# Performance work log

Measured on AMD Instinct MI355X. Metric: run time of the kernel, lower is better.

## Reference

```python
import jax, jax.numpy as jnp
import numpy as np

ROPE_BASE = 100.0  # CroCo RoPE2D default freq


def _rope1d(tok, pos):
    # tok: [B, H, N, D], pos: [B, N] int
    D = tok.shape[-1]
    inv_freq = 1.0 / (ROPE_BASE ** (jnp.arange(0, D, 2, dtype=jnp.float32) / D))
    ang = pos[..., None].astype(jnp.float32) * inv_freq          # [B, N, D/2]
    cos = jnp.concatenate([jnp.cos(ang), jnp.cos(ang)], -1)[:, None]  # [B,1,N,D]
    sin = jnp.concatenate([jnp.sin(ang), jnp.sin(ang)], -1)[:, None]
    x1, x2 = jnp.split(tok, 2, axis=-1)
    rot = jnp.concatenate([-x2, x1], -1)
    return tok * cos.astype(tok.dtype) + rot * sin.astype(tok.dtype)


def _rope2d(tok, pos):
    # first half of head channels rotated with y coords, second half with x
    t_y, t_x = jnp.split(tok, 2, axis=-1)
    return jnp.concatenate([_rope1d(t_y, pos[..., 0]), _rope1d(t_x, pos[..., 1])], -1)


def setup_inputs() -> dict:
    key0 = jax.random.key(0)
    ks = jax.random.split(key0, 10)
    B, Nq, Nk, C, H = 4, 2048, 2048, 1024, 16
    s = 1.0 / np.sqrt(C)
    return {
        "query": jax.random.normal(ks[0], (B, Nq, C), jnp.float32),
        "key": jax.random.normal(ks[1], (B, Nk, C), jnp.float32),
        "value": jax.random.normal(ks[2], (B, Nk, C), jnp.float32),
        "qpos": jax.random.randint(ks[3], (B, Nq, 2), 0, 64),
        "kpos": jax.random.randint(ks[4], (B, Nk, 2), 0, 64),
        "Wq": jax.random.normal(ks[5], (C, C), jnp.float32) * s,
        "Wk": jax.random.normal(ks[6], (C, C), jnp.float32) * s,
        "Wv": jax.random.normal(ks[7], (C, C), jnp.float32) * s,
        "Wo": jax.random.normal(ks[8], (C, C), jnp.float32) * s,
        "bo": jax.random.normal(ks[9], (C,), jnp.float32) * 0.01,
    }


def reference(query, key, value, qpos, kpos, Wq, Wk, Wv, Wo, bo):
    B, Nq, C = query.shape
    H = 16
    D = C // H
    scale = D ** (-0.5)
    # separate Q/K/V projections (torch Linear: x @ W.T), split into heads
    q = (query @ Wq.T).reshape(B, Nq, H, D).transpose(0, 2, 1, 3)
    k = (key @ Wk.T).reshape(B, key.shape[1], H, D).transpose(0, 2, 1, 3)
    v = (value @ Wv.T).reshape(B, value.shape[1], H, D).transpose(0, 2, 1, 3)
    # inline fp16 cast around RoPE, as in the original
    q = _rope2d(q.astype(jnp.float16), qpos).astype(jnp.float32)
    k = _rope2d(k.astype(jnp.float16), kpos).astype(jnp.float32)
    # SDPA
    scores = jnp.einsum("bhqd,bhkd->bhqk", q, k) * scale
    attn = jax.nn.softmax(scores, axis=-1)
    x = jnp.einsum("bhqk,bhkd->bhqd", attn, v)
    x = x.transpose(0, 2, 1, 3).reshape(B, Nq, C)
    return x @ Wo.T + bo
```

## Files before the change

kernel.cpp:

```cpp
#include <hip/hip_runtime.h>
#include <math.h>

typedef _Float16 half_t;
typedef __attribute__((ext_vector_type(8))) _Float16 f16x8;
typedef __attribute__((ext_vector_type(4))) float f32x4;

#define MFMA16(a, b, c) __builtin_amdgcn_mfma_f32_16x16x32_f16((a), (b), (c), 0, 0, 0)

constexpr int Bc = 4, NQ = 2048, NKC = 2048, CC = 1024, NHD = 16, HDIM = 64;

__device__ __forceinline__ void async_copy16(half_t* lds, const half_t* g) {
  __builtin_amdgcn_global_load_lds(
      (const __attribute__((address_space(1))) unsigned*)g,
      (__attribute__((address_space(3))) unsigned*)lds, 16, 0, 0);
}

__global__ __launch_bounds__(256) void cvt16(const float* __restrict__ src,
                                             half_t* __restrict__ dst) {
  const int i = blockIdx.x * 256 + threadIdx.x;
  const f32x4 a = ((const f32x4*)src)[2 * i];
  const f32x4 b = ((const f32x4*)src)[2 * i + 1];
  f16x8 h;
#pragma unroll
  for (int j = 0; j < 4; ++j) { h[j] = (half_t)a[j]; h[4 + j] = (half_t)b[j]; }
  ((f16x8*)dst)[i] = h;
}

__global__ __launch_bounds__(256) void cvtW(const float* __restrict__ s0,
                                            const float* __restrict__ s1,
                                            const float* __restrict__ s2,
                                            const float* __restrict__ s3,
                                            half_t* __restrict__ dst) {
  const int y = blockIdx.y;
  const float* src = (y == 0) ? s0 : (y == 1) ? s1 : (y == 2) ? s2 : s3;
  const int i = blockIdx.x * 256 + threadIdx.x;
  const f32x4 a = ((const f32x4*)src)[2 * i];
  const f32x4 b = ((const f32x4*)src)[2 * i + 1];
  f16x8 h;
#pragma unroll
  for (int j = 0; j < 4; ++j) { h[j] = (half_t)a[j]; h[4 + j] = (half_t)b[j]; }
  ((f16x8*)(dst + (size_t)y * CC * CC))[i] = h;
}

template <bool FINAL>
__global__ __launch_bounds__(256) void gemm_lds(const half_t* __restrict__ X,
                                                const half_t* __restrict__ W,
                                                half_t* __restrict__ out16,
                                                float* __restrict__ outf,
                                                const float* __restrict__ bias) {
  __shared__ half_t As[128 * 32];
  __shared__ half_t Bs[128 * 32];
  const int tid  = threadIdx.x;
  const int wave = tid >> 6, lane = tid & 63;
  const int quad = lane >> 4, l16 = lane & 15;
  const int m0 = blockIdx.y * 128, n0 = blockIdx.x * 128;
  const int mw = (wave >> 1) * 64, nw = (wave & 1) * 64;

  const int srow = lane >> 2, skoff = (lane & 3) * 8;
  const half_t* xa = X + (size_t)(m0 + wave * 32 + srow) * CC + skoff;
  const half_t* xb = W + (size_t)(n0 + wave * 32 + srow) * CC + skoff;
  half_t* lA0 = &As[(wave * 2 + 0) * 512];
  half_t* lA1 = &As[(wave * 2 + 1) * 512];
  half_t* lB0 = &Bs[(wave * 2 + 0) * 512];
  half_t* lB1 = &Bs[(wave * 2 + 1) * 512];

  f32x4 acc[4][4] = {};

  for (int k0 = 0; k0 < CC; k0 += 32) {
    __syncthreads();
    async_copy16(lA0, xa + k0);
    async_copy16(lA1, xa + 16 * CC + k0);
    async_copy16(lB0, xb + k0);
    async_copy16(lB1, xb + 16 * CC + k0);
    __syncthreads();

    f16x8 af[4], bf[4];
#pragma unroll
    for (int mi = 0; mi < 4; ++mi) af[mi] = *(const f16x8*)&As[(mw + mi * 16 + l16) * 32 + quad * 8];
#pragma unroll
    for (int ni = 0; ni < 4; ++ni) bf[ni] = *(const f16x8*)&Bs[(nw + ni * 16 + l16) * 32 + quad * 8];
#pragma unroll
    for (int mi = 0; mi < 4; ++mi)
#pragma unroll
      for (int ni = 0; ni < 4; ++ni) acc[mi][ni] = MFMA16(af[mi], bf[ni], acc[mi][ni]);
  }

#pragma unroll
  for (int mi = 0; mi < 4; ++mi)
#pragma unroll
    for (int ni = 0; ni < 4; ++ni)
#pragma unroll
      for (int r = 0; r < 4; ++r) {
        const size_t row = (size_t)(m0 + mw + mi * 16 + quad * 4 + r);
        const size_t col = (size_t)(n0 + nw + ni * 16 + l16);
        if constexpr (FINAL) outf[row * CC + col] = acc[mi][ni][r] + bias[col];
        else                 out16[row * CC + col] = (half_t)acc[mi][ni][r];
      }
}

__global__ __launch_bounds__(256) void rope_kernel(half_t* __restrict__ t,
                                                   const int* __restrict__ pos) {
#pragma clang fp contract(off)
  const int gid = blockIdx.x * 256 + threadIdx.x;
  const int i       = gid & 15;
  const int halfsel = (gid >> 4) & 1;
  const int h       = (gid >> 5) & 15;
  const int n       = (gid >> 9) & 2047;
  const int b       = gid >> 20;

  const int p = pos[((b * NQ + n) << 1) + halfsel];
  const float inv = __builtin_amdgcn_exp2f((float)i * -0.41524100904865773f);
  const float ang = (float)p * inv;
  const half_t hc = (half_t)cosf(ang);
  const half_t hs = (half_t)sinf(ang);

  const size_t base = (size_t)(b * NQ + n) * CC + h * HDIM + halfsel * 32;
  const half_t t1 = t[base + i];
  const half_t t2 = t[base + 16 + i];
  const half_t p1 = t1 * hc;
  const half_t p2 = t2 * hs;
  const half_t p3 = t2 * hc;
  const half_t p4 = t1 * hs;
  t[base + i]      = p1 - p2;
  t[base + 16 + i] = p3 + p4;
}

__global__ __launch_bounds__(256, 4) void attn_kernel(const half_t* __restrict__ q16,
                                                      const half_t* __restrict__ k16,
                                                      const half_t* __restrict__ v16,
                                                      half_t* __restrict__ x16) {
  __shared__ half_t Ksf[4 * 64 * 16];
  __shared__ half_t Vt[64][72];
  __shared__ half_t Pl[4][32][72];
  const int tid  = threadIdx.x;
  const int wave = tid >> 6, lane = tid & 63;
  const int quad = lane >> 4, l16 = lane & 15;
  const int qblk = blockIdx.x, h = blockIdx.y, b = blockIdx.z;
  const f32x4 zero = {0.f, 0.f, 0.f, 0.f};

  f16x8 qa[2][2];
  {
    const half_t* qbase =
        q16 + (size_t)(b * NQ + qblk * 128 + wave * 32 + l16) * CC + h * HDIM + quad * 8;
#pragma unroll
    for (int mi = 0; mi < 2; ++mi)
#pragma unroll
      for (int kc = 0; kc < 2; ++kc)
        qa[mi][kc] = *(const f16x8*)(qbase + (size_t)mi * 16 * CC + kc * 32);
  }

  f32x4 o[2][4] = {};
  f32x4 lp[2] = {};

  const int skey = tid >> 2, sd0 = (tid & 3) * 16;
  const int vp = tid & 31, vd0 = (tid >> 5) * 8;
  const half_t* kptr = k16 + (size_t)(b * NKC + skey) * CC + h * HDIM + sd0;
  const half_t* vptr = v16 + (size_t)(b * NKC + 2 * vp) * CC + h * HDIM + vd0;

  int kdst[2];
#pragma unroll
  for (int c = 0; c < 2; ++c) {
    const int d = sd0 + 8 * c;
    const int nb = skey >> 4, kc = d >> 5, qd = (d & 31) >> 3;
    const int slot = (skey & 15) + 16 * qd;
    kdst[c] = (nb * 64 + slot) * 16 + kc * 8;
  }

  f16x8 kr0, kr1, vr0, vr1;
  kr0 = *(const f16x8*)kptr;
  kr1 = *(const f16x8*)(kptr + 8);
  vr0 = *(const f16x8*)vptr;
  vr1 = *(const f16x8*)(vptr + CC);

  for (int kt = 0; kt < NKC; kt += 64) {
    __syncthreads();
    *(f16x8*)&Ksf[kdst[0]] = kr0;
    *(f16x8*)&Ksf[kdst[1]] = kr1;
#pragma unroll
    for (int i = 0; i < 8; ++i) {
      union { half_t h2[2]; unsigned u; } pk;
      pk.h2[0] = vr0[i]; pk.h2[1] = vr1[i];
      *(unsigned*)&Vt[vd0 + i][2 * vp] = pk.u;
    }
    __syncthreads();

    if (kt + 64 < NKC) {
      const half_t* kn = kptr + (size_t)(kt + 64) * CC;
      const half_t* vn = vptr + (size_t)(kt + 64) * CC;
      kr0 = *(const f16x8*)kn;
      kr1 = *(const f16x8*)(kn + 8);
      vr0 = *(const f16x8*)vn;
      vr1 = *(const f16x8*)(vn + CC);
    }

    f32x4 s[2][4];
#pragma unroll
    for (int nb = 0; nb < 4; ++nb) {
      const f16x8 kb0 = *(const f16x8*)&Ksf[(nb * 64 + lane) * 16 + 0];
      const f16x8 kb1 = *(const f16x8*)&Ksf[(nb * 64 + lane) * 16 + 8];
#pragma unroll
      for (int mi = 0; mi < 2; ++mi) {
        const f32x4 t0 = MFMA16(qa[mi][0], kb0, zero);
        s[mi][nb] = MFMA16(qa[mi][1], kb1, t0);
      }
    }

#pragma unroll
    for (int mi = 0; mi < 2; ++mi)
#pragma unroll
      for (int nb = 0; nb < 4; ++nb)
#pragma unroll
        for (int r = 0; r < 4; ++r) {
          const float p = __builtin_amdgcn_exp2f(s[mi][nb][r] * 0.18033688011112042f);
          s[mi][nb][r] = p;
          lp[mi][r] += p;
        }

#pragma unroll
    for (int mi = 0; mi < 2; ++mi)
#pragma unroll
      for (int nb = 0; nb < 4; ++nb)
#pragma unroll
        for (int r = 0; r < 4; ++r)
          Pl[wave][mi * 16 + quad * 4 + r][nb * 16 + l16] = (half_t)s[mi][nb][r];

#pragma unroll
    for (int kc = 0; kc < 2; ++kc) {
      const f16x8 pa0 = *(const f16x8*)&Pl[wave][l16][kc * 32 + quad * 8];
      const f16x8 pa1 = *(const f16x8*)&Pl[wave][16 + l16][kc * 32 + quad * 8];
#pragma unroll
      for (int nd = 0; nd < 4; ++nd) {
        const f16x8 vb = *(const f16x8*)&Vt[nd * 16 + l16][kc * 32 + quad * 8];
        o[0][nd] = MFMA16(pa0, vb, o[0][nd]);
        o[1][nd] = MFMA16(pa1, vb, o[1][nd]);
      }
    }
  }

#pragma unroll
  for (int mi = 0; mi < 2; ++mi)
#pragma unroll
    for (int r = 0; r < 4; ++r) {
      float rs = lp[mi][r];
#pragma unroll
      for (int off = 1; off < 16; off <<= 1) rs += __shfl_xor(rs, off);
      const float inv = 1.f / rs;
      const size_t row =
          (size_t)(b * NQ + qblk * 128 + wave * 32 + mi * 16 + quad * 4 + r) * CC + h * HDIM;
#pragma unroll
      for (int nd = 0; nd < 4; ++nd)
        x16[row + nd * 16 + l16] = (half_t)(o[mi][nd][r] * inv);
    }
}

extern "C" void kernel_launch(void* const* d_in, const int* in_sizes, int n_in,
                              void* d_out, int out_size, void* d_ws, size_t ws_size,
                              hipStream_t stream) {
  const float* query = (const float*)d_in[0];
  const float* key   = (const float*)d_in[1];
  const float* value = (const float*)d_in[2];
  const int*   qpos  = (const int*)d_in[3];
  const int*   kpos  = (const int*)d_in[4];
  const float* Wq = (const float*)d_in[5];
  const float* Wk = (const float*)d_in[6];
  const float* Wv = (const float*)d_in[7];
  const float* Wo = (const float*)d_in[8];
  const float* bo = (const float*)d_in[9];
  float* out = (float*)d_out;

  const size_t NT = (size_t)Bc * NQ * CC;
  half_t* q16 = (half_t*)d_ws;
  half_t* k16 = q16 + NT;
  half_t* v16 = k16 + NT;
  half_t* A0  = v16 + NT;
  half_t* W16 = A0 + NT;
  half_t* x16 = A0;

  const int nbA = (int)(NT / 8 / 256);
  const int nbW = (CC * CC) / 8 / 256;

  cvtW<<<dim3(nbW, 4), 256, 0, stream>>>(Wq, Wk, Wv, Wo, W16);

  const dim3 gg(CC / 128, Bc * NQ / 128);
  cvt16<<<nbA, 256, 0, stream>>>(query, A0);
  gemm_lds<false><<<gg, 256, 0, stream>>>(A0, W16 + 0 * (size_t)CC * CC, q16, nullptr, nullptr);
  cvt16<<<nbA, 256, 0, stream>>>(key, A0);
  gemm_lds<false><<<gg, 256, 0, stream>>>(A0, W16 + 1 * (size_t)CC * CC, k16, nullptr, nullptr);
  cvt16<<<nbA, 256, 0, stream>>>(value, A0);
  gemm_lds<false><<<gg, 256, 0, stream>>>(A0, W16 + 2 * (size_t)CC * CC, v16, nullptr, nullptr);

  rope_kernel<<<(Bc * NQ * NHD * 32) / 256, 256, 0, stream>>>(q16, qpos);
  rope_kernel<<<(Bc * NQ * NHD * 32) / 256, 256, 0, stream>>>(k16, kpos);

  attn_kernel<<<dim3(NQ / 128, NHD, Bc), 256, 0, stream>>>(q16, k16, v16, x16);

  gemm_lds<true><<<gg, 256, 0, stream>>>(x16, W16 + 3 * (size_t)CC * CC, nullptr, out, bo);
}
```

Measured before the change: 409.2 us.

## Fuse fp32 input conversion into batched QKV GEMM and restructure attention tiling

The three QKV projections now run as a single GEMM launch over blockIdx.z and convert fp32 activations to fp16 while staging them into LDS, which removes the separate cvt16 passes and their round trips through global memory. Blocks are remapped to a grouped tile order for better L2 reuse, and the two RoPE launches are merged into one. The attention kernel now processes 128 keys per iteration with transposed MFMA operands (K·Q and V·P). It also uses a swizzled LDS layout for P and vectorized f16x4 stores, and drops the occupancy hint of 4 blocks per CU. In exchange, the fp32 A loads go through registers instead of the async LDS path, and the larger per-iteration register tile may cut occupancy.

```diff
diff --git a/kernel.cpp b/kernel.cpp
--- a/kernel.cpp
+++ b/kernel.cpp
@@ -3,6 +3,7 @@
 
 typedef _Float16 half_t;
 typedef __attribute__((ext_vector_type(8))) _Float16 f16x8;
+typedef __attribute__((ext_vector_type(4))) _Float16 f16x4;
 typedef __attribute__((ext_vector_type(4))) float f32x4;
 
 #define MFMA16(a, b, c) __builtin_amdgcn_mfma_f32_16x16x32_f16((a), (b), (c), 0, 0, 0)
@@ -13,17 +14,6 @@
   __builtin_amdgcn_global_load_lds(
       (const __attribute__((address_space(1))) unsigned*)g,
       (__attribute__((address_space(3))) unsigned*)lds, 16, 0, 0);
-}
-
-__global__ __launch_bounds__(256) void cvt16(const float* __restrict__ src,
-                                             half_t* __restrict__ dst) {
-  const int i = blockIdx.x * 256 + threadIdx.x;
-  const f32x4 a = ((const f32x4*)src)[2 * i];
-  const f32x4 b = ((const f32x4*)src)[2 * i + 1];
-  f16x8 h;
-#pragma unroll
-  for (int j = 0; j < 4; ++j) { h[j] = (half_t)a[j]; h[4 + j] = (half_t)b[j]; }
-  ((f16x8*)dst)[i] = h;
 }
 
 __global__ __launch_bounds__(256) void cvtW(const float* __restrict__ s0,
@@ -42,36 +32,64 @@
   ((f16x8*)(dst + (size_t)y * CC * CC))[i] = h;
 }
 
-template <bool FINAL>
-__global__ __launch_bounds__(256) void gemm_lds(const half_t* __restrict__ X,
-                                                const half_t* __restrict__ W,
-                                                half_t* __restrict__ out16,
-                                                float* __restrict__ outf,
-                                                const float* __restrict__ bias) {
+template <bool QKV>
+__global__ __launch_bounds__(256) void gemm_k(const float* __restrict__ X0,
+                                              const float* __restrict__ X1,
+                                              const float* __restrict__ X2,
+                                              const half_t* __restrict__ Xh,
+                                              const half_t* __restrict__ W16,
+                                              half_t* __restrict__ o0,
+                                              half_t* __restrict__ o1,
+                                              half_t* __restrict__ o2,
+                                              float* __restrict__ outf,
+                                              const float* __restrict__ bias) {
   __shared__ half_t As[128 * 32];
   __shared__ half_t Bs[128 * 32];
-  const int tid  = threadIdx.x;
-  const int wave = tid >> 6, lane = tid & 63;
+  const int tid = threadIdx.x, wave = tid >> 6, lane = tid & 63;
   const int quad = lane >> 4, l16 = lane & 15;
-  const int m0 = blockIdx.y * 128, n0 = blockIdx.x * 128;
+  const int z = QKV ? blockIdx.z : 3;
+  const int idx = blockIdx.y * 8 + blockIdx.x;
+  const int rb = (idx & 7) | ((idx >> 6) << 3);
+  const int cb = (idx >> 3) & 7;
+  const int m0 = rb * 128, n0 = cb * 128;
   const int mw = (wave >> 1) * 64, nw = (wave & 1) * 64;
 
-  const int srow = lane >> 2, skoff = (lane & 3) * 8;
-  const half_t* xa = X + (size_t)(m0 + wave * 32 + srow) * CC + skoff;
-  const half_t* xb = W + (size_t)(n0 + wave * 32 + srow) * CC + skoff;
-  half_t* lA0 = &As[(wave * 2 + 0) * 512];
-  half_t* lA1 = &As[(wave * 2 + 1) * 512];
-  half_t* lB0 = &Bs[(wave * 2 + 0) * 512];
-  half_t* lB1 = &Bs[(wave * 2 + 1) * 512];
+  const float* Xf = QKV ? (z == 0 ? X0 : z == 1 ? X1 : X2) : nullptr;
+  const half_t* Wz = W16 + (size_t)z * CC * CC;
+
+  const int arow = (lane >> 2), acol = (lane & 3) * 8;
+  const int srow = tid >> 1, sc16 = (tid & 1) * 16;
 
   f32x4 acc[4][4] = {};
 
   for (int k0 = 0; k0 < CC; k0 += 32) {
     __syncthreads();
-    async_copy16(lA0, xa + k0);
-    async_copy16(lA1, xa + 16 * CC + k0);
-    async_copy16(lB0, xb + k0);
-    async_copy16(lB1, xb + 16 * CC + k0);
+    if constexpr (QKV) {
+      const float* xp = Xf + (size_t)(m0 + srow) * CC + k0 + sc16;
+      const f32x4 x0 = *(const f32x4*)xp;
+      const f32x4 x1 = *(const f32x4*)(xp + 4);
+      const f32x4 x2 = *(const f32x4*)(xp + 8);
+      const f32x4 x3 = *(const f32x4*)(xp + 12);
+      f16x8 h0, h1;
+#pragma unroll
+      for (int j = 0; j < 4; ++j) {
+        h0[j] = (half_t)x0[j]; h0[4 + j] = (half_t)x1[j];
+        h1[j] = (half_t)x2[j]; h1[4 + j] = (half_t)x3[j];
+      }
+      *(f16x8*)&As[srow * 32 + sc16]     = h0;
+      *(f16x8*)&As[srow * 32 + sc16 + 8] = h1;
+    } else {
+#pragma unroll
+      for (int c = 0; c < 2; ++c) {
+        const int br = (wave * 2 + c) * 16;
+        async_copy16(&As[br * 32], Xh + (size_t)(m0 + br + arow) * CC + k0 + acol);
+      }
+    }
+#pragma unroll
+    for (int c = 0; c < 2; ++c) {
+      const int br = (wave * 2 + c) * 16;
+      async_copy16(&Bs[br * 32], Wz + (size_t)(n0 + br + arow) * CC + k0 + acol);
+    }
     __syncthreads();
 
     f16x8 af[4], bf[4];
@@ -85,22 +103,36 @@
       for (int ni = 0; ni < 4; ++ni) acc[mi][ni] = MFMA16(af[mi], bf[ni], acc[mi][ni]);
   }
 
-#pragma unroll
-  for (int mi = 0; mi < 4; ++mi)
-#pragma unroll
-    for (int ni = 0; ni < 4; ++ni)
-#pragma unroll
-      for (int r = 0; r < 4; ++r) {
-        const size_t row = (size_t)(m0 + mw + mi * 16 + quad * 4 + r);
-        const size_t col = (size_t)(n0 + nw + ni * 16 + l16);
-        if constexpr (FINAL) outf[row * CC + col] = acc[mi][ni][r] + bias[col];
-        else                 out16[row * CC + col] = (half_t)acc[mi][ni][r];
-      }
-}
-
-__global__ __launch_bounds__(256) void rope_kernel(half_t* __restrict__ t,
-                                                   const int* __restrict__ pos) {
+  if constexpr (QKV) {
+    half_t* out16 = z == 0 ? o0 : z == 1 ? o1 : o2;
+#pragma unroll
+    for (int mi = 0; mi < 4; ++mi)
+#pragma unroll
+      for (int ni = 0; ni < 4; ++ni)
+#pragma unroll
+        for (int r = 0; r < 4; ++r)
+          out16[(size_t)(m0 + mw + mi * 16 + quad * 4 + r) * CC + n0 + nw + ni * 16 + l16] =
+              (half_t)acc[mi][ni][r];
+  } else {
+#pragma unroll
+    for (int mi = 0; mi < 4; ++mi)
+#pragma unroll
+      for (int ni = 0; ni < 4; ++ni)
+#pragma unroll
+        for (int r = 0; r < 4; ++r) {
+          const int col = n0 + nw + ni * 16 + l16;
+          outf[(size_t)(m0 + mw + mi * 16 + quad * 4 + r) * CC + col] = acc[mi][ni][r] + bias[col];
+        }
+  }
+}
+
+__global__ __launch_bounds__(256) void rope2(half_t* __restrict__ tq,
+                                             half_t* __restrict__ tk,
+                                             const int* __restrict__ qpos,
+                                             const int* __restrict__ kpos) {
 #pragma clang fp contract(off)
+  half_t* t = blockIdx.y ? tk : tq;
+  const int* pos = blockIdx.y ? kpos : qpos;
   const int gid = blockIdx.x * 256 + threadIdx.x;
   const int i       = gid & 15;
   const int halfsel = (gid >> 4) & 1;
@@ -125,15 +157,14 @@
   t[base + 16 + i] = p3 + p4;
 }
 
-__global__ __launch_bounds__(256, 4) void attn_kernel(const half_t* __restrict__ q16,
-                                                      const half_t* __restrict__ k16,
-                                                      const half_t* __restrict__ v16,
-                                                      half_t* __restrict__ x16) {
-  __shared__ half_t Ksf[4 * 64 * 16];
-  __shared__ half_t Vt[64][72];
-  __shared__ half_t Pl[4][32][72];
-  const int tid  = threadIdx.x;
-  const int wave = tid >> 6, lane = tid & 63;
+__global__ __launch_bounds__(256) void attn_kernel(const half_t* __restrict__ q16,
+                                                   const half_t* __restrict__ k16,
+                                                   const half_t* __restrict__ v16,
+                                                   half_t* __restrict__ x16) {
+  __shared__ half_t Ksf[2 * 8 * 64 * 8];
+  __shared__ half_t Vsf[4 * 4 * 64 * 8];
+  __shared__ half_t Pt[4][2][16 * 64];
+  const int tid = threadIdx.x, wave = tid >> 6, lane = tid & 63;
   const int quad = lane >> 4, l16 = lane & 15;
   const int qblk = blockIdx.x, h = blockIdx.y, b = blockIdx.z;
   const f32x4 zero = {0.f, 0.f, 0.f, 0.f};
@@ -150,107 +181,103 @@
   }
 
   f32x4 o[2][4] = {};
-  f32x4 lp[2] = {};
-
-  const int skey = tid >> 2, sd0 = (tid & 3) * 16;
-  const int vp = tid & 31, vd0 = (tid >> 5) * 8;
-  const half_t* kptr = k16 + (size_t)(b * NKC + skey) * CC + h * HDIM + sd0;
-  const half_t* vptr = v16 + (size_t)(b * NKC + 2 * vp) * CC + h * HDIM + vd0;
-
-  int kdst[2];
-#pragma unroll
-  for (int c = 0; c < 2; ++c) {
-    const int d = sd0 + 8 * c;
-    const int nb = skey >> 4, kc = d >> 5, qd = (d & 31) >> 3;
-    const int slot = (skey & 15) + 16 * qd;
-    kdst[c] = (nb * 64 + slot) * 16 + kc * 8;
-  }
-
-  f16x8 kr0, kr1, vr0, vr1;
-  kr0 = *(const f16x8*)kptr;
-  kr1 = *(const f16x8*)(kptr + 8);
-  vr0 = *(const f16x8*)vptr;
-  vr1 = *(const f16x8*)(vptr + CC);
-
-  for (int kt = 0; kt < NKC; kt += 64) {
+  float lp[2] = {0.f, 0.f};
+
+  const int sk = tid >> 1, kcs = tid & 1;
+  const half_t* kptr = k16 + (size_t)(b * NKC + sk) * CC + h * HDIM + kcs * 32;
+  const int kdst = ((kcs * 8 + (sk >> 4)) * 64 + (sk & 15)) * 8;
+  const int s_ = tid & 63, d0v = (tid >> 6) * 16;
+  const half_t* vptr = v16 + (size_t)(b * NKC + 2 * s_) * CC + h * HDIM + d0v;
+  const int vbase = (((s_ >> 4) * 4 + (d0v >> 4)) * 64 + 16 * ((s_ >> 2) & 3)) * 8 + 2 * (s_ & 3);
+
+  f16x8 kr[4], vr[4];
+#pragma unroll
+  for (int g = 0; g < 4; ++g) kr[g] = *(const f16x8*)(kptr + 8 * g);
+  vr[0] = *(const f16x8*)vptr;        vr[1] = *(const f16x8*)(vptr + 8);
+  vr[2] = *(const f16x8*)(vptr + CC); vr[3] = *(const f16x8*)(vptr + CC + 8);
+
+  for (int kt = 0; kt < NKC; kt += 128) {
     __syncthreads();
-    *(f16x8*)&Ksf[kdst[0]] = kr0;
-    *(f16x8*)&Ksf[kdst[1]] = kr1;
+#pragma unroll
+    for (int g = 0; g < 4; ++g) *(f16x8*)&Ksf[kdst + 128 * g] = kr[g];
 #pragma unroll
     for (int i = 0; i < 8; ++i) {
-      union { half_t h2[2]; unsigned u; } pk;
-      pk.h2[0] = vr0[i]; pk.h2[1] = vr1[i];
-      *(unsigned*)&Vt[vd0 + i][2 * vp] = pk.u;
+      union { half_t h2[2]; unsigned u; } pa, pb;
+      pa.h2[0] = vr[0][i]; pa.h2[1] = vr[2][i];
+      pb.h2[0] = vr[1][i]; pb.h2[1] = vr[3][i];
+      *(unsigned*)&Vsf[vbase + i * 8]       = pa.u;
+      *(unsigned*)&Vsf[vbase + (8 + i) * 8] = pb.u;
     }
     __syncthreads();
 
-    if (kt + 64 < NKC) {
-      const half_t* kn = kptr + (size_t)(kt + 64) * CC;
-      const half_t* vn = vptr + (size_t)(kt + 64) * CC;
-      kr0 = *(const f16x8*)kn;
-      kr1 = *(const f16x8*)(kn + 8);
-      vr0 = *(const f16x8*)vn;
-      vr1 = *(const f16x8*)(vn + CC);
-    }
-
-    f32x4 s[2][4];
-#pragma unroll
-    for (int nb = 0; nb < 4; ++nb) {
-      const f16x8 kb0 = *(const f16x8*)&Ksf[(nb * 64 + lane) * 16 + 0];
-      const f16x8 kb1 = *(const f16x8*)&Ksf[(nb * 64 + lane) * 16 + 8];
-#pragma unroll
-      for (int mi = 0; mi < 2; ++mi) {
-        const f32x4 t0 = MFMA16(qa[mi][0], kb0, zero);
-        s[mi][nb] = MFMA16(qa[mi][1], kb1, t0);
+    if (kt + 128 < NKC) {
+      const half_t* kn = kptr + (size_t)(kt + 128) * CC;
+      const half_t* vn = vptr + (size_t)(kt + 128) * CC;
+#pragma unroll
+      for (int g = 0; g < 4; ++g) kr[g] = *(const f16x8*)(kn + 8 * g);
+      vr[0] = *(const f16x8*)vn;        vr[1] = *(const f16x8*)(vn + 8);
+      vr[2] = *(const f16x8*)(vn + CC); vr[3] = *(const f16x8*)(vn + CC + 8);
+    }
+
+#pragma unroll
+    for (int hh = 0; hh < 2; ++hh) {
+      f32x4 s[2][4];
+#pragma unroll
+      for (int nbl = 0; nbl < 4; ++nbl) {
+        const int nb = hh * 4 + nbl;
+        const f16x8 kb0 = *(const f16x8*)&Ksf[(nb * 64 + lane) * 8];
+        const f16x8 kb1 = *(const f16x8*)&Ksf[((8 + nb) * 64 + lane) * 8];
+#pragma unroll
+        for (int mi = 0; mi < 2; ++mi) {
+          const f32x4 t0 = MFMA16(kb0, qa[mi][0], zero);
+          s[mi][nbl] = MFMA16(kb1, qa[mi][1], t0);
+        }
       }
-    }
-
-#pragma unroll
-    for (int mi = 0; mi < 2; ++mi)
-#pragma unroll
-      for (int nb = 0; nb < 4; ++nb)
-#pragma unroll
-        for (int r = 0; r < 4; ++r) {
-          const float p = __builtin_amdgcn_exp2f(s[mi][nb][r] * 0.18033688011112042f);
-          s[mi][nb][r] = p;
-          lp[mi][r] += p;
+#pragma unroll
+      for (int mi = 0; mi < 2; ++mi)
+#pragma unroll
+        for (int nbl = 0; nbl < 4; ++nbl) {
+          f16x4 pk;
+#pragma unroll
+          for (int r = 0; r < 4; ++r) {
+            const float p = __builtin_amdgcn_exp2f(s[mi][nbl][r] * 0.18033688011112042f);
+            lp[mi] += p;
+            pk[r] = (half_t)p;
+          }
+          const int Cw = (2 * nbl + (quad >> 1)) ^ (l16 & 7);
+          *(f16x4*)&Pt[wave][mi][l16 * 64 + Cw * 8 + (quad & 1) * 4] = pk;
         }
-
-#pragma unroll
-    for (int mi = 0; mi < 2; ++mi)
-#pragma unroll
-      for (int nb = 0; nb < 4; ++nb)
-#pragma unroll
-        for (int r = 0; r < 4; ++r)
-          Pl[wave][mi * 16 + quad * 4 + r][nb * 16 + l16] = (half_t)s[mi][nb][r];
-
-#pragma unroll
-    for (int kc = 0; kc < 2; ++kc) {
-      const f16x8 pa0 = *(const f16x8*)&Pl[wave][l16][kc * 32 + quad * 8];
-      const f16x8 pa1 = *(const f16x8*)&Pl[wave][16 + l16][kc * 32 + quad * 8];
-#pragma unroll
-      for (int nd = 0; nd < 4; ++nd) {
-        const f16x8 vb = *(const f16x8*)&Vt[nd * 16 + l16][kc * 32 + quad * 8];
-        o[0][nd] = MFMA16(pa0, vb, o[0][nd]);
-        o[1][nd] = MFMA16(pa1, vb, o[1][nd]);
+#pragma unroll
+      for (int kkl = 0; kkl < 2; ++kkl) {
+        const int kk = hh * 2 + kkl;
+        const int Cr = (kkl * 4 + quad) ^ (l16 & 7);
+        const f16x8 pb0 = *(const f16x8*)&Pt[wave][0][l16 * 64 + Cr * 8];
+        const f16x8 pb1 = *(const f16x8*)&Pt[wave][1][l16 * 64 + Cr * 8];
+#pragma unroll
+        for (int md = 0; md < 4; ++md) {
+          const f16x8 va = *(const f16x8*)&Vsf[((kk * 4 + md) * 64 + lane) * 8];
+          o[0][md] = MFMA16(va, pb0, o[0][md]);
+          o[1][md] = MFMA16(va, pb1, o[1][md]);
+        }
       }
     }
   }
 
 #pragma unroll
-  for (int mi = 0; mi < 2; ++mi)
-#pragma unroll
-    for (int r = 0; r < 4; ++r) {
-      float rs = lp[mi][r];
-#pragma unroll
-      for (int off = 1; off < 16; off <<= 1) rs += __shfl_xor(rs, off);
-      const float inv = 1.f / rs;
-      const size_t row =
-          (size_t)(b * NQ + qblk * 128 + wave * 32 + mi * 16 + quad * 4 + r) * CC + h * HDIM;
-#pragma unroll
-      for (int nd = 0; nd < 4; ++nd)
-        x16[row + nd * 16 + l16] = (half_t)(o[mi][nd][r] * inv);
-    }
+  for (int mi = 0; mi < 2; ++mi) {
+    float rs = lp[mi];
+    rs += __shfl_xor(rs, 16);
+    rs += __shfl_xor(rs, 32);
+    const float inv = 1.f / rs;
+    const size_t qrow = (size_t)(b * NQ + qblk * 128 + wave * 32 + mi * 16 + l16);
+#pragma unroll
+    for (int md = 0; md < 4; ++md) {
+      f16x4 pk;
+#pragma unroll
+      for (int r = 0; r < 4; ++r) pk[r] = (half_t)(o[mi][md][r] * inv);
+      *(f16x4*)&x16[qrow * CC + h * HDIM + md * 16 + quad * 4] = pk;
+    }
+  }
 }
 
 extern "C" void kernel_launch(void* const* d_in, const int* in_sizes, int n_in,
@@ -272,27 +299,18 @@
   half_t* q16 = (half_t*)d_ws;
   half_t* k16 = q16 + NT;
   half_t* v16 = k16 + NT;
-  half_t* A0  = v16 + NT;
-  half_t* W16 = A0 + NT;
-  half_t* x16 = A0;
-
-  const int nbA = (int)(NT / 8 / 256);
-  const int nbW = (CC * CC) / 8 / 256;
-
-  cvtW<<<dim3(nbW, 4), 256, 0, stream>>>(Wq, Wk, Wv, Wo, W16);
-
-  const dim3 gg(CC / 128, Bc * NQ / 128);
-  cvt16<<<nbA, 256, 0, stream>>>(query, A0);
-  gemm_lds<false><<<gg, 256, 0, stream>>>(A0, W16 + 0 * (size_t)CC * CC, q16, nullptr, nullptr);
-  cvt16<<<nbA, 256, 0, stream>>>(key, A0);
-  gemm_lds<false><<<gg, 256, 0, stream>>>(A0, W16 + 1 * (size_t)CC * CC, k16, nullptr, nullptr);
-  cvt16<<<nbA, 256, 0, stream>>>(value, A0);
-  gemm_lds<false><<<gg, 256, 0, stream>>>(A0, W16 + 2 * (size_t)CC * CC, v16, nullptr, nullptr);
-
-  rope_kernel<<<(Bc * NQ * NHD * 32) / 256, 256, 0, stream>>>(q16, qpos);
-  rope_kernel<<<(Bc * NQ * NHD * 32) / 256, 256, 0, stream>>>(k16, kpos);
+  half_t* x16 = v16 + NT;
+  half_t* W16 = x16 + NT;
+
+  cvtW<<<dim3((CC * CC) / 8 / 256, 4), 256, 0, stream>>>(Wq, Wk, Wv, Wo, W16);
+
+  gemm_k<true><<<dim3(8, 64, 3), 256, 0, stream>>>(query, key, value, nullptr, W16,
+                                                   q16, k16, v16, nullptr, nullptr);
+
+  rope2<<<dim3((Bc * NQ * NHD * 32) / 256, 2), 256, 0, stream>>>(q16, k16, qpos, kpos);
 
   attn_kernel<<<dim3(NQ / 128, NHD, Bc), 256, 0, stream>>>(q16, k16, v16, x16);
 
-  gemm_lds<true><<<gg, 256, 0, stream>>>(x16, W16 + 3 * (size_t)CC * CC, nullptr, out, bo);
-}
+  gemm_k<false><<<dim3(8, 64), 256, 0, stream>>>(nullptr, nullptr, nullptr, x16, W16,
+                                                 nullptr, nullptr, nullptr, out, bo);
+}
```

Result: no change. 416.7 us (+1.8%).
